# Optimization experiments

Measured on AMD Instinct MI355X. Metric: run time of the kernel, lower is better.

## Reference

```python
import jax, jax.numpy as jnp
import numpy as np
import math

E = 1024   # embedding_dim
H = 16     # num_attention_heads
DH = 64    # head_embedding_dim
THD = H * DH
EPS = 1e-5

def _layernorm(x, g, b):
    m = jnp.mean(x, axis=-1, keepdims=True)
    v = jnp.mean(jnp.square(x - m), axis=-1, keepdims=True)
    return (x - m) * jax.lax.rsqrt(v + EPS) * g + b

def setup_inputs() -> dict:
    key = jax.random.key(0)
    ks = jax.random.split(key, 16)
    s_in = 1.0 / math.sqrt(E)
    s_o = 1.0 / math.sqrt(THD)
    inp = {"tokens": jax.random.normal(ks[0], (2, 2048, E), dtype=jnp.float32)}
    # q_linear / k_linear / v_linear: LayerNorm(E) then Linear(E -> THD)
    for i, name in enumerate(["q", "k", "v"]):
        inp[f"ln_{name}_g"] = jnp.ones((E,), jnp.float32)
        inp[f"ln_{name}_b"] = jnp.zeros((E,), jnp.float32)
        inp[f"W{name}"] = jax.random.uniform(ks[1 + 2 * i], (E, THD), jnp.float32, -s_in, s_in)
        inp[f"b{name}"] = jax.random.uniform(ks[2 + 2 * i], (THD,), jnp.float32, -s_in, s_in)
    # attention_linear: LayerNorm(THD) then Linear(THD -> E)
    inp["ln_o_g"] = jnp.ones((THD,), jnp.float32)
    inp["ln_o_b"] = jnp.zeros((THD,), jnp.float32)
    inp["Wo"] = jax.random.uniform(ks[7], (THD, E), jnp.float32, -s_o, s_o)
    inp["bo"] = jax.random.uniform(ks[8], (E,), jnp.float32, -s_o, s_o)
    return inp

def reference(tokens, ln_q_g, ln_q_b, Wq, bq, ln_k_g, ln_k_b, Wk, bk,
              ln_v_g, ln_v_b, Wv, bv, ln_o_g, ln_o_b, Wo, bo):
    N, L, _ = tokens.shape
    # NOTE: faithful to source quirk -- k comes from v_linear, v comes from k_linear.
    q = (_layernorm(tokens, ln_q_g, ln_q_b) @ Wq + bq).reshape(N, L, H, DH).transpose(0, 2, 1, 3)  # (N,H,L,Dh)
    k = (_layernorm(tokens, ln_v_g, ln_v_b) @ Wv + bv).reshape(N, L, H, DH).transpose(0, 2, 3, 1)  # (N,H,Dh,L)
    v = (_layernorm(tokens, ln_k_g, ln_k_b) @ Wk + bk).reshape(N, L, H, DH).transpose(0, 2, 1, 3)  # (N,H,L,Dh)
    qkT = jnp.einsum('bhid,bhdj->bhij', q, k)  # (N,H,L,L)
    # mask added BEFORE dividing by sqrt(Dh), as in source
    mask = jnp.triu(jnp.full((L, L), -9999.0, dtype=qkT.dtype), k=1)
    attn = jax.nn.softmax((qkT + mask) / math.sqrt(DH), axis=-1)
    wv = jnp.einsum('bhij,bhjd->bhid', attn, v).transpose(0, 2, 1, 3).reshape(N, L, THD)
    out = _layernorm(wv, ln_o_g, ln_o_b) @ Wo + bo + tokens
    return (out, k, v)
```

## Files before the change

kernel.cpp:

```cpp
#include <hip/hip_runtime.h>

#define L_SEQ 2048
#define NH    16
#define E_DIM 1024
#define M_ROWS 4096

typedef unsigned short u16;
typedef unsigned int   u32;
typedef __attribute__((ext_vector_type(8))) __bf16 bf16x8;
typedef __attribute__((ext_vector_type(4))) float  f32x4;

__device__ __forceinline__ u16 f2bf(float f) {
  union { float f; u32 u; } x; x.f = f;
  u32 u = x.u;
  return (u16)((u + 0x7FFFu + ((u >> 16) & 1u)) >> 16);
}
__device__ __forceinline__ float bf2f(u16 v) {
  union { u32 u; float f; } x; x.u = ((u32)v) << 16;
  return x.f;
}
__device__ __forceinline__ void st_bf4(u16* p, float a, float b, float c, float d) {
  ushort4 u; u.x = f2bf(a); u.y = f2bf(b); u.z = f2bf(c); u.w = f2bf(d);
  *reinterpret_cast<ushort4*>(p) = u;
}
__device__ __forceinline__ void gload16(const u16* g, u16* l) {
  __builtin_amdgcn_global_load_lds(
      (const __attribute__((address_space(1))) void*)g,
      (__attribute__((address_space(3))) void*)l, 16, 0, 0);
}
#define SBAR() asm volatile("s_barrier" ::: "memory")

__global__ __launch_bounds__(256) void ln_hat_f32(const float* __restrict__ x, u16* __restrict__ o)
{
  __shared__ float red[8];
  const size_t row = blockIdx.x;
  const int t = threadIdx.x;
  float4 v = reinterpret_cast<const float4*>(x + row * E_DIM)[t];
  float s = v.x + v.y + v.z + v.w;
  float q = v.x*v.x + v.y*v.y + v.z*v.z + v.w*v.w;
  #pragma unroll
  for (int off = 32; off; off >>= 1) { s += __shfl_down(s, off); q += __shfl_down(q, off); }
  if ((t & 63) == 0) { red[t >> 6] = s; red[4 + (t >> 6)] = q; }
  __syncthreads();
  float S = red[0] + red[1] + red[2] + red[3];
  float Q = red[4] + red[5] + red[6] + red[7];
  float mean = S * (1.f / E_DIM);
  float rstd = rsqrtf(Q * (1.f / E_DIM) - mean * mean + 1e-5f);
  st_bf4(o + row * E_DIM + t * 4,
         (v.x - mean) * rstd, (v.y - mean) * rstd, (v.z - mean) * rstd, (v.w - mean) * rstd);
}

__global__ __launch_bounds__(256) void ln_hat_bf16(const u16* __restrict__ x, u16* __restrict__ o)
{
  __shared__ float red[8];
  const size_t row = blockIdx.x;
  const int t = threadIdx.x;
  ushort4 u = reinterpret_cast<const ushort4*>(x + row * E_DIM)[t];
  float v0 = bf2f(u.x), v1 = bf2f(u.y), v2 = bf2f(u.z), v3 = bf2f(u.w);
  float s = v0 + v1 + v2 + v3;
  float q = v0*v0 + v1*v1 + v2*v2 + v3*v3;
  #pragma unroll
  for (int off = 32; off; off >>= 1) { s += __shfl_down(s, off); q += __shfl_down(q, off); }
  if ((t & 63) == 0) { red[t >> 6] = s; red[4 + (t >> 6)] = q; }
  __syncthreads();
  float S = red[0] + red[1] + red[2] + red[3];
  float Q = red[4] + red[5] + red[6] + red[7];
  float mean = S * (1.f / E_DIM);
  float rstd = rsqrtf(Q * (1.f / E_DIM) - mean * mean + 1e-5f);
  st_bf4(o + row * E_DIM + t * 4,
         (v0 - mean) * rstd, (v1 - mean) * rstd, (v2 - mean) * rstd, (v3 - mean) * rstd);
}

__global__ __launch_bounds__(256) void transpose_all(
    const float* __restrict__ W0, const float* __restrict__ W1,
    const float* __restrict__ W2, const float* __restrict__ W3,
    const float* __restrict__ g0, const float* __restrict__ g1,
    const float* __restrict__ g2, const float* __restrict__ g3,
    u16* __restrict__ T0, u16* __restrict__ T1, u16* __restrict__ T2, u16* __restrict__ T3)
{
  __shared__ float tile[32][33];
  const int z = blockIdx.z;
  const float* W = (z == 0) ? W0 : (z == 1) ? W1 : (z == 2) ? W2 : W3;
  const float* g = (z == 0) ? g0 : (z == 1) ? g1 : (z == 2) ? g2 : g3;
  u16* T = (z == 0) ? T0 : (z == 1) ? T1 : (z == 2) ? T2 : T3;
  const int tx = threadIdx.x & 31, ty = threadIdx.x >> 5;
  const int bx = blockIdx.x * 32, by = blockIdx.y * 32;
  #pragma unroll
  for (int r = 0; r < 4; ++r) {
    const int e = by + ty + r * 8;
    tile[ty + r * 8][tx] = W[(size_t)e * E_DIM + bx + tx] * g[e];
  }
  __syncthreads();
  #pragma unroll
  for (int r = 0; r < 4; ++r)
    T[(size_t)(bx + ty + r * 8) * E_DIM + by + tx] = f2bf(tile[tx][ty + r * 8]);
}

__global__ __launch_bounds__(256) void bias_fold(
    const float* __restrict__ W0, const float* __restrict__ W1,
    const float* __restrict__ W2, const float* __restrict__ W3,
    const float* __restrict__ l0, const float* __restrict__ l1,
    const float* __restrict__ l2, const float* __restrict__ l3,
    const float* __restrict__ b0, const float* __restrict__ b1,
    const float* __restrict__ b2, const float* __restrict__ b3,
    float* __restrict__ bfold)
{
  __shared__ float part[8][32];
  const int z = blockIdx.y;
  const float* W  = (z == 0) ? W0 : (z == 1) ? W1 : (z == 2) ? W2 : W3;
  const float* bl = (z == 0) ? l0 : (z == 1) ? l1 : (z == 2) ? l2 : l3;
  const float* bs = (z == 0) ? b0 : (z == 1) ? b1 : (z == 2) ? b2 : b3;
  const int tn = threadIdx.x & 31, te = threadIdx.x >> 5;
  const int n = blockIdx.x * 32 + tn;
  float acc = 0.f;
  const int e0 = te * 128;
  for (int e = e0; e < e0 + 128; ++e) acc += bl[e] * W[(size_t)e * E_DIM + n];
  part[te][tn] = acc;
  __syncthreads();
  if (te == 0) {
    float s = part[0][tn] + part[1][tn] + part[2][tn] + part[3][tn]
            + part[4][tn] + part[5][tn] + part[6][tn] + part[7][tn];
    bfold[z * E_DIM + n] = bs[n] + s;
  }
}

#define GBK 64
__device__ __forceinline__ void core128(
    const u16* __restrict__ A, const u16* __restrict__ BT,
    int m0, int n0, int t, u16* lds, f32x4 (&acc)[4][4])
{
  const int lane = t & 63, wave = t >> 6;
  const int wm = wave >> 1, wn = wave & 1;
  const int fr = lane & 15, hi = lane >> 4;
  const int sx = fr & 7;

  auto STAGE = [&](int buf, int kt) {
    u16* la = lds + (buf * 2 + 0) * (128 * GBK);
    u16* lb = lds + (buf * 2 + 1) * (128 * GBK);
    #pragma unroll
    for (int s = 0; s < 4; ++s) {
      const int seg = t + s * 256;
      const int r = seg >> 3;
      const int gc = (seg & 7) ^ (r & 7);
      gload16(A + (size_t)(m0 + r) * E_DIM + kt * GBK + gc * 8, la + seg * 8);
    }
    #pragma unroll
    for (int s = 0; s < 4; ++s) {
      const int seg = t + s * 256;
      const int r = seg >> 3;
      const int gc = (seg & 7) ^ (r & 7);
      gload16(BT + (size_t)(n0 + r) * E_DIM + kt * GBK + gc * 8, lb + seg * 8);
    }
  };
  auto AF = [&](int buf, int i, int ks) -> bf16x8 {
    return *reinterpret_cast<const bf16x8*>(
        lds + (buf * 2 + 0) * (128 * GBK) + (wm * 64 + i * 16 + fr) * GBK + (((ks * 4 + hi) ^ sx) * 8));
  };
  auto BF = [&](int buf, int j, int ks) -> bf16x8 {
    return *reinterpret_cast<const bf16x8*>(
        lds + (buf * 2 + 1) * (128 * GBK) + (wn * 64 + j * 16 + fr) * GBK + (((ks * 4 + hi) ^ sx) * 8));
  };
  auto PHASES = [&](int buf) {
    bf16x8 a[4][2], b[4][2];
    #pragma unroll
    for (int i = 0; i < 4; ++i) { a[i][0] = AF(buf, i, 0); a[i][1] = AF(buf, i, 1); }
    #pragma unroll
    for (int j = 0; j < 4; ++j) { b[j][0] = BF(buf, j, 0); b[j][1] = BF(buf, j, 1); }
    __builtin_amdgcn_s_setprio(1);
    #pragma unroll
    for (int i = 0; i < 4; ++i)
      #pragma unroll
      for (int j = 0; j < 4; ++j) {
        acc[i][j] = __builtin_amdgcn_mfma_f32_16x16x32_bf16(a[i][0], b[j][0], acc[i][j], 0, 0, 0);
        acc[i][j] = __builtin_amdgcn_mfma_f32_16x16x32_bf16(a[i][1], b[j][1], acc[i][j], 0, 0, 0);
      }
    __builtin_amdgcn_s_setprio(0);
  };

  STAGE(0, 0);
  #pragma unroll 1
  for (int kt = 0; kt < 15; ++kt) {
    const int buf = kt & 1;
    SBAR();
    STAGE(buf ^ 1, kt + 1);
    asm volatile("s_waitcnt vmcnt(8)" ::: "memory");
    SBAR();
    PHASES(buf);
  }
  asm volatile("s_waitcnt vmcnt(0)" ::: "memory");
  SBAR();
  PHASES(1);
}

__global__ __launch_bounds__(256, 2) void gemm_qkv128(
    const u16* __restrict__ xhat, const u16* __restrict__ WTcat,
    const float* __restrict__ bfold,
    float* __restrict__ kout, float* __restrict__ vout,
    u16* __restrict__ qbf, u16* __restrict__ kbf, u16* __restrict__ vTb)
{
  __shared__ u16 lds[4 * 128 * GBK];
  const int t = threadIdx.x;
  const int sw = (blockIdx.x & 7) * 96 + (blockIdx.x >> 3);
  const int by = sw / 24, bx = sw % 24;
  const int m0 = by * 128, n0 = bx * 128;

  f32x4 acc[4][4] = {};
  core128(xhat, WTcat, m0, n0, t, lds, acc);

  const int lane = t & 63, wave = t >> 6;
  const int wm = wave >> 1, wn = wave & 1;
  const int fr = lane & 15, hi = lane >> 4;
  const int z = n0 >> 10;
  const float* bias = bfold + z * E_DIM;
  const int rowb = hi * 4;
  #pragma unroll
  for (int i = 0; i < 4; ++i) {
    const int mbase = m0 + wm * 64 + i * 16 + rowb;
    #pragma unroll
    for (int j = 0; j < 4; ++j) {
      const int ng = n0 + wn * 64 + j * 16 + fr;
      const int ncol = ng & 1023;
      const float bval = bias[ncol];
      #pragma unroll
      for (int r = 0; r < 4; ++r) {
        const int m = mbase + r;
        const float val = acc[i][j][r] + bval;
        const int b = m >> 11, l = m & 2047, h = ncol >> 6, d = ncol & 63;
        const size_t bh = (size_t)(b * NH + h);
        if (z == 0) {
          qbf[((bh * L_SEQ + l) << 6) + d] = f2bf(val);
        } else if (z == 1) {
          kout[(bh * 64 + d) * L_SEQ + l] = val;
          kbf[((bh * L_SEQ + l) << 6) + d] = f2bf(val);
        } else {
          vout[(bh * L_SEQ + l) * 64 + d] = val;
          vTb[(bh * 64 + d) * L_SEQ + l] = f2bf(val);
        }
      }
    }
  }
}

__global__ __launch_bounds__(256, 2) void gemm_o128(
    const u16* __restrict__ A, const u16* __restrict__ BT, const float* __restrict__ bias,
    const float* __restrict__ tokens, float* __restrict__ out)
{
  __shared__ u16 lds[4 * 128 * GBK];
  const int t = threadIdx.x;
  const int sw = (blockIdx.x & 7) * 32 + (blockIdx.x >> 3);
  const int by = sw / 8, bx = sw % 8;
  const int m0 = by * 128, n0 = bx * 128;

  f32x4 acc[4][4] = {};
  core128(A, BT, m0, n0, t, lds, acc);

  const int lane = t & 63, wave = t >> 6;
  const int wm = wave >> 1, wn = wave & 1;
  const int fr = lane & 15, hi = lane >> 4;
  const int rowb = hi * 4;
  #pragma unroll
  for (int i = 0; i < 4; ++i) {
    const int mbase = m0 + wm * 64 + i * 16 + rowb;
    #pragma unroll
    for (int j = 0; j < 4; ++j) {
      const int ncol = n0 + wn * 64 + j * 16 + fr;
      const float bval = bias[ncol];
      #pragma unroll
      for (int r = 0; r < 4; ++r) {
        const int m = mbase + r;
        out[(size_t)m * E_DIM + ncol] = acc[i][j][r] + bval + tokens[(size_t)m * E_DIM + ncol];
      }
    }
  }
}

__global__ __launch_bounds__(256) void attn_mfma(
    const u16* __restrict__ qbf, const u16* __restrict__ kbf,
    const u16* __restrict__ vTb, u16* __restrict__ wv)
{
  __shared__ u16 Klds[64][72];
  __shared__ u16 Vlds[64][72];
  __shared__ u16 Plds[4][16][72];
  const int t = threadIdx.x, lane = t & 63, wave = t >> 6;
  const int bi = blockIdx.x;
  const int bh = (bi & 7) + 8 * ((bi >> 3) & 3);
  const int pr = bi >> 5;
  const int fr = lane & 15, hi = lane >> 4;
  const u16* kbase = kbf + (size_t)bh * L_SEQ * 64;
  const u16* vbase = vTb + (size_t)bh * 64 * L_SEQ;
  const int b = bh >> 4, h = bh & 15;

  #pragma unroll 1
  for (int half = 0; half < 2; ++half) {
    const int qt = half ? (31 - pr) : pr;
    const int q0w = qt * 64 + wave * 16;
    const int qg = q0w + fr;

    const u16* qrow = qbf + ((size_t)bh * L_SEQ + q0w + fr) * 64 + hi * 8;
    const bf16x8 qf0 = *reinterpret_cast<const bf16x8*>(qrow);
    const bf16x8 qf1 = *reinterpret_cast<const bf16x8*>(qrow + 32);

    f32x4 o[4] = {};
    float mrun = -3.0e38f, lrun = 0.f;

    for (int tkv = 0; tkv <= qt; ++tkv) {
      const int j0 = tkv * 64;
      const bool diag = (tkv == qt);
      #pragma unroll
      for (int s = 0; s < 2; ++s) {
        const int seg = t + s * 256;
        const int r = seg >> 3, c8 = (seg & 7) * 8;
        *reinterpret_cast<uint4*>(&Klds[r][c8]) =
            *reinterpret_cast<const uint4*>(kbase + (size_t)(j0 + r) * 64 + c8);
        *reinterpret_cast<uint4*>(&Vlds[r][c8]) =
            *reinterpret_cast<const uint4*>(vbase + (size_t)r * L_SEQ + j0 + c8);
      }
      __syncthreads();

      f32x4 st[4] = {};
      __builtin_amdgcn_s_setprio(1);
      #pragma unroll
      for (int kt = 0; kt < 4; ++kt) {
        bf16x8 ka0 = *reinterpret_cast<const bf16x8*>(&Klds[kt*16 + fr][hi*8]);
        bf16x8 ka1 = *reinterpret_cast<const bf16x8*>(&Klds[kt*16 + fr][32 + hi*8]);
        st[kt] = __builtin_amdgcn_mfma_f32_16x16x32_bf16(ka0, qf0, st[kt], 0, 0, 0);
        st[kt] = __builtin_amdgcn_mfma_f32_16x16x32_bf16(ka1, qf1, st[kt], 0, 0, 0);
      }
      __builtin_amdgcn_s_setprio(0);

      float p[16];
      float pmax = -3.0e38f;
      #pragma unroll
      for (int kt = 0; kt < 4; ++kt)
        #pragma unroll
        for (int r = 0; r < 4; ++r) {
          const int key = j0 + kt*16 + hi*4 + r;
          const float v = st[kt][r] * 0.125f +
                          ((diag && key > qg) ? -1249.875f : 0.f);
          p[kt*4 + r] = v;
          pmax = fmaxf(pmax, v);
        }
      pmax = fmaxf(pmax, __shfl_xor(pmax, 16));
      pmax = fmaxf(pmax, __shfl_xor(pmax, 32));
      const float mnew = fmaxf(mrun, pmax);
      const float alpha = __expf(mrun - mnew);
      float lsum = 0.f;
      #pragma unroll
      for (int i = 0; i < 16; ++i) { p[i] = __expf(p[i] - mnew); lsum += p[i]; }
      lsum += __shfl_xor(lsum, 16);
      lsum += __shfl_xor(lsum, 32);
      lrun = lrun * alpha + lsum;
      mrun = mnew;
      #pragma unroll
      for (int r = 0; r < 4; ++r) {
        const float ar = __shfl(alpha, hi*4 + r);
        o[0][r] *= ar; o[1][r] *= ar; o[2][r] *= ar; o[3][r] *= ar;
      }

      #pragma unroll
      for (int kt = 0; kt < 4; ++kt) {
        ushort4 w4;
        w4.x = f2bf(p[kt*4+0]); w4.y = f2bf(p[kt*4+1]);
        w4.z = f2bf(p[kt*4+2]); w4.w = f2bf(p[kt*4+3]);
        *reinterpret_cast<ushort4*>(&Plds[wave][fr][kt*16 + hi*4]) = w4;
      }

      const bf16x8 pf0 = *reinterpret_cast<const bf16x8*>(&Plds[wave][fr][hi*8]);
      const bf16x8 pf1 = *reinterpret_cast<const bf16x8*>(&Plds[wave][fr][32 + hi*8]);
      __builtin_amdgcn_s_setprio(1);
      #pragma unroll
      for (int dt = 0; dt < 4; ++dt) {
        bf16x8 vf0 = *reinterpret_cast<const bf16x8*>(&Vlds[dt*16 + fr][hi*8]);
        bf16x8 vf1 = *reinterpret_cast<const bf16x8*>(&Vlds[dt*16 + fr][32 + hi*8]);
        o[dt] = __builtin_amdgcn_mfma_f32_16x16x32_bf16(pf0, vf0, o[dt], 0, 0, 0);
        o[dt] = __builtin_amdgcn_mfma_f32_16x16x32_bf16(pf1, vf1, o[dt], 0, 0, 0);
      }
      __builtin_amdgcn_s_setprio(0);
      __syncthreads();
    }

    const float inv = 1.f / lrun;
    #pragma unroll
    for (int r = 0; r < 4; ++r) {
      const float ir = __shfl(inv, hi*4 + r);
      const int q = q0w + hi*4 + r;
      u16* dst = wv + (size_t)(b * L_SEQ + q) * E_DIM + h * 64 + fr;
      #pragma unroll
      for (int dt = 0; dt < 4; ++dt)
        dst[dt * 16] = f2bf(o[dt][r] * ir);
    }
  }
}

extern "C" void kernel_launch(void* const* d_in, const int* in_sizes, int n_in,
                              void* d_out, int out_size, void* d_ws, size_t ws_size,
                              hipStream_t stream) {
  (void)in_sizes; (void)n_in; (void)out_size; (void)ws_size;
  const float* tokens = (const float*)d_in[0];
  const float* ln_q_g = (const float*)d_in[1];
  const float* ln_q_b = (const float*)d_in[2];
  const float* Wq     = (const float*)d_in[3];
  const float* bq     = (const float*)d_in[4];
  const float* ln_k_g = (const float*)d_in[5];
  const float* ln_k_b = (const float*)d_in[6];
  const float* Wk     = (const float*)d_in[7];
  const float* bk     = (const float*)d_in[8];
  const float* ln_v_g = (const float*)d_in[9];
  const float* ln_v_b = (const float*)d_in[10];
  const float* Wv     = (const float*)d_in[11];
  const float* bv     = (const float*)d_in[12];
  const float* ln_o_g = (const float*)d_in[13];
  const float* ln_o_b = (const float*)d_in[14];
  const float* Wo     = (const float*)d_in[15];
  const float* bo     = (const float*)d_in[16];

  float* out  = (float*)d_out;
  float* kout = out + 4194304;
  float* vout = kout + 4194304;

  char* w = (char*)d_ws;
  const size_t MB = (size_t)1 << 20;
  u16*   WTq   = (u16*)(w + 0 * MB);
  u16*   WTv   = (u16*)(w + 2 * MB);
  u16*   WTk   = (u16*)(w + 4 * MB);
  u16*   WTo   = (u16*)(w + 6 * MB);
  u16*   xhat  = (u16*)(w + 8 * MB);
  u16*   qbf   = (u16*)(w + 16 * MB);
  u16*   kbf   = (u16*)(w + 24 * MB);
  u16*   vTb   = (u16*)(w + 32 * MB);
  u16*   what  = (u16*)(w + 40 * MB);
  float* bfold = (float*)(w + 48 * MB);
  u16*   wvb   = xhat;

  transpose_all<<<dim3(32, 32, 4), 256, 0, stream>>>(
      Wq, Wv, Wk, Wo, ln_q_g, ln_v_g, ln_k_g, ln_o_g, WTq, WTv, WTk, WTo);
  bias_fold<<<dim3(32, 4), 256, 0, stream>>>(
      Wq, Wv, Wk, Wo, ln_q_b, ln_v_b, ln_k_b, ln_o_b, bq, bv, bk, bo, bfold);
  ln_hat_f32<<<M_ROWS, 256, 0, stream>>>(tokens, xhat);
  gemm_qkv128<<<768, 256, 0, stream>>>(xhat, WTq, bfold, kout, vout, qbf, kbf, vTb);
  attn_mfma<<<512, 256, 0, stream>>>(qbf, kbf, vTb, wvb);
  ln_hat_bf16<<<M_ROWS, 256, 0, stream>>>(wvb, what);
  gemm_o128<<<256, 256, 0, stream>>>(what, WTo, bfold + 3 * E_DIM, tokens, out);
}
```

Baseline: 142.7 us.

## Stage transposed K/V epilogue stores through LDS and remap XCD tile blocks

The QKV GEMM epilogue now writes the transposed fp32 K output and the bf16 V^T output into a padded shared-memory tile first. It then emits them as contiguous 16-byte vector stores, replacing scattered strided scalar stores. Block-to-tile mapping in both GEMMs is also changed so each XCD covers a compact 2D patch of tiles, which should improve L2 reuse. The cost is extra LDS traffic and barriers in the epilogue, plus a larger shared buffer that could reduce occupancy.

```diff
diff --git a/kernel.cpp b/kernel.cpp
--- a/kernel.cpp
+++ b/kernel.cpp
@@ -198,10 +198,12 @@
     float* __restrict__ kout, float* __restrict__ vout,
     u16* __restrict__ qbf, u16* __restrict__ kbf, u16* __restrict__ vTb)
 {
-  __shared__ u16 lds[4 * 128 * GBK];
+  __shared__ __align__(16) char smraw[128 * 132 * 4];
+  u16* lds = (u16*)smraw;
   const int t = threadIdx.x;
-  const int sw = (blockIdx.x & 7) * 96 + (blockIdx.x >> 3);
-  const int by = sw / 24, bx = sw % 24;
+  const int xcd = blockIdx.x & 7, l = blockIdx.x >> 3;
+  const int by = 8 * (xcd >> 1) + l / 12;
+  const int bx = 12 * (xcd & 1) + l % 12;
   const int m0 = by * 128, n0 = bx * 128;
 
   f32x4 acc[4][4] = {};
@@ -213,31 +215,89 @@
   const int z = n0 >> 10;
   const float* bias = bfold + z * E_DIM;
   const int rowb = hi * 4;
-  #pragma unroll
-  for (int i = 0; i < 4; ++i) {
-    const int mbase = m0 + wm * 64 + i * 16 + rowb;
-    #pragma unroll
-    for (int j = 0; j < 4; ++j) {
-      const int ng = n0 + wn * 64 + j * 16 + fr;
-      const int ncol = ng & 1023;
-      const float bval = bias[ncol];
-      #pragma unroll
-      for (int r = 0; r < 4; ++r) {
-        const int m = mbase + r;
-        const float val = acc[i][j][r] + bval;
-        const int b = m >> 11, l = m & 2047, h = ncol >> 6, d = ncol & 63;
-        const size_t bh = (size_t)(b * NH + h);
-        if (z == 0) {
-          qbf[((bh * L_SEQ + l) << 6) + d] = f2bf(val);
-        } else if (z == 1) {
-          kout[(bh * 64 + d) * L_SEQ + l] = val;
-          kbf[((bh * L_SEQ + l) << 6) + d] = f2bf(val);
-        } else {
-          vout[(bh * L_SEQ + l) * 64 + d] = val;
-          vTb[(bh * 64 + d) * L_SEQ + l] = f2bf(val);
+  const int bb = m0 >> 11;
+
+  if (z == 0) {
+    #pragma unroll
+    for (int i = 0; i < 4; ++i) {
+      const int mbase = m0 + wm * 64 + i * 16 + rowb;
+      #pragma unroll
+      for (int j = 0; j < 4; ++j) {
+        const int ncol = (n0 + wn * 64 + j * 16 + fr) & 1023;
+        const float bval = bias[ncol];
+        const int h = ncol >> 6, d = ncol & 63;
+        #pragma unroll
+        for (int r = 0; r < 4; ++r) {
+          const int m = mbase + r;
+          const int ltok = m & 2047;
+          qbf[(((size_t)(bb * NH + h) * L_SEQ + ltok) << 6) + d] = f2bf(acc[i][j][r] + bval);
         }
       }
     }
+  } else if (z == 1) {
+    __syncthreads();
+    float (*xp)[132] = (float(*)[132])smraw;
+    #pragma unroll
+    for (int i = 0; i < 4; ++i) {
+      const int mbase = m0 + wm * 64 + i * 16 + rowb;
+      const int mloc = wm * 64 + i * 16 + rowb;
+      #pragma unroll
+      for (int j = 0; j < 4; ++j) {
+        const int nl = wn * 64 + j * 16 + fr;
+        const int ncol = (n0 + nl) & 1023;
+        const float bval = bias[ncol];
+        const int h = ncol >> 6, d = ncol & 63;
+        #pragma unroll
+        for (int r = 0; r < 4; ++r) {
+          const int m = mbase + r;
+          const int ltok = m & 2047;
+          const float val = acc[i][j][r] + bval;
+          kbf[(((size_t)(bb * NH + h) * L_SEQ + ltok) << 6) + d] = f2bf(val);
+          xp[nl][mloc + r] = val;
+        }
+      }
+    }
+    __syncthreads();
+    const int nl = t >> 1, mh = (t & 1) * 64;
+    const int ncol2 = (n0 + nl) & 1023;
+    const int h2 = ncol2 >> 6, d2 = ncol2 & 63;
+    float4* dst = (float4*)(kout + ((size_t)(bb * NH + h2) * 64 + d2) * L_SEQ + (m0 & 2047) + mh);
+    #pragma unroll
+    for (int u = 0; u < 16; ++u)
+      dst[u] = *reinterpret_cast<float4*>(&xp[nl][mh + u * 4]);
+  } else {
+    __syncthreads();
+    u32 (*vp)[68] = (u32(*)[68])smraw;
+    #pragma unroll
+    for (int i = 0; i < 4; ++i) {
+      const int mbase = m0 + wm * 64 + i * 16 + rowb;
+      const int mloc = wm * 64 + i * 16 + rowb;
+      #pragma unroll
+      for (int j = 0; j < 4; ++j) {
+        const int nl = wn * 64 + j * 16 + fr;
+        const int ncol = (n0 + nl) & 1023;
+        const float bval = bias[ncol];
+        const int h = ncol >> 6, d = ncol & 63;
+        float v4[4];
+        #pragma unroll
+        for (int r = 0; r < 4; ++r) {
+          const int m = mbase + r;
+          const int ltok = m & 2047;
+          v4[r] = acc[i][j][r] + bval;
+          vout[((size_t)(bb * NH + h) * L_SEQ + ltok) * 64 + d] = v4[r];
+        }
+        vp[nl][(mloc >> 1) + 0] = (u32)f2bf(v4[0]) | ((u32)f2bf(v4[1]) << 16);
+        vp[nl][(mloc >> 1) + 1] = (u32)f2bf(v4[2]) | ((u32)f2bf(v4[3]) << 16);
+      }
+    }
+    __syncthreads();
+    const int nl = t >> 1, mh = (t & 1) * 64;
+    const int ncol2 = (n0 + nl) & 1023;
+    const int h2 = ncol2 >> 6, d2 = ncol2 & 63;
+    uint4* dst = (uint4*)(vTb + ((size_t)(bb * NH + h2) * 64 + d2) * L_SEQ + (m0 & 2047) + mh);
+    #pragma unroll
+    for (int u = 0; u < 8; ++u)
+      dst[u] = *reinterpret_cast<uint4*>(&vp[nl][(mh >> 1) + u * 4]);
   }
 }
 
@@ -247,8 +307,9 @@
 {
   __shared__ u16 lds[4 * 128 * GBK];
   const int t = threadIdx.x;
-  const int sw = (blockIdx.x & 7) * 32 + (blockIdx.x >> 3);
-  const int by = sw / 8, bx = sw % 8;
+  const int xcd = blockIdx.x & 7, l = blockIdx.x >> 3;
+  const int by = 8 * (xcd >> 1) + (l >> 2);
+  const int bx = 4 * (xcd & 1) + (l & 3);
   const int m0 = by * 128, n0 = bx * 128;
 
   f32x4 acc[4][4] = {};
```

Result: faster. 129.8 us (-9.1%).
